# Performance work log

Hardware: AMD Instinct MI355X
Metric: run time of the kernel (lower is better)

The kernel has to match this reference:

```python
import jax, jax.numpy as jnp
import numpy as np

SHIFTS = (1, 2, 4, 8)


def _base_kernels():
    # 8 directional contrast kernels (center minus one neighbor), as in the torch module
    d1 = np.array([[[-1, 0, 0], [0, 1, 0], [0, 0, 0]],
                   [[0, -1, 0], [0, 1, 0], [0, 0, 0]],
                   [[0, 0, -1], [0, 1, 0], [0, 0, 0]],
                   [[0, 0, 0], [0, 1, -1], [0, 0, 0]]], dtype=np.float32)
    d2 = d1[:, ::-1, ::-1].copy()
    delta = np.concatenate([d1, d2], axis=0)            # (8,3,3) kernel*_1
    su0 = np.ones((3, 3), np.float32) / 8.0             # original kernel_su
    ce = np.zeros((3, 3), np.float32); ce[1, 1] = 1.0   # kernel_ce
    k2 = (delta - ce) * (9.0 / 8.0) + su0               # (8,3,3) kernel*_2
    su_f = su0 * (7.0 / 8.0); su_f[1, 1] = 1.0 / 8.0    # mutated kernel_su used for cen_x
    return jnp.asarray(delta), jnp.asarray(k2), jnp.asarray(su_f), jnp.asarray(ce)


def _dwconv(x, w, dil, groups):
    # depthwise 3x3 dilated conv, padding='same' (stride 1)
    return jax.lax.conv_general_dilated(
        x, w, window_strides=(1, 1), padding='SAME',
        rhs_dilation=(dil, dil),
        dimension_numbers=('NCHW', 'OIHW', 'NCHW'),
        feature_group_count=groups)


def setup_inputs() -> dict:
    key = jax.random.key(0)
    ks = jax.random.split(key, 6)
    B, C, Wd, Ht = 8, 16, 192, 192
    H, T, OC = 4, 64, 32
    hid = T // H  # 16
    return {
        'cen': jax.random.normal(ks[0], (B, C, Wd, Ht), jnp.float32),
        'wq': jax.random.normal(ks[1], (H, hid, C), jnp.float32) * 0.1,
        'wk': jax.random.normal(ks[2], (H, 8 * hid, 8 * C), jnp.float32) * 0.05,
        'wv': jax.random.normal(ks[3], (H, 8 * hid, 8 * C), jnp.float32) * 0.05,
        'sum_w': jnp.full((H, C), 0.5, jnp.float32),  # Parameter(ones)*0.5
        'w_out': jax.random.normal(ks[4], (OC, T), jnp.float32) * 0.1,
        'gamma': jnp.ones((OC,), jnp.float32),
        'beta': jnp.zeros((OC,), jnp.float32),
    }


def reference(cen, wq, wk, wv, sum_w, w_out, gamma, beta):
    delta, k2, su_f, ce = _base_kernels()
    B, C, Wd, Ht = cen.shape
    H = len(SHIFTS)
    hid = wq.shape[1]
    N = Wd * Ht  # self.area
    qs, ks_, vs = [], [], []
    for i, s in enumerate(SHIFTS):
        sw = sum_w[i]  # (C,) per-channel blend weight
        # center-smoothing kernel: kernel_su*(1-sw) + sw*kernel_ce
        w_cen = (su_f[None] * (1.0 - sw)[:, None, None]
                 + ce[None] * sw[:, None, None])[:, None]          # (C,1,3,3)
        cen_x = _dwconv(cen, w_cen, s, C)                           # (B,C,Wd,Ht)
        # 8 blended contrast kernels: k1*(1-sw) + k2*sw, per channel
        w_sur = (delta[None] * (1.0 - sw)[:, None, None, None]
                 + k2[None] * sw[:, None, None, None]).reshape(C * 8, 1, 3, 3)
        sur = _dwconv(cen, w_sur, s, C)                             # (B, C*8, Wd, Ht), channel-major
        # reorder to torch cat order: [k0 all C, k1 all C, ...]
        sur = sur.reshape(B, C, 8, Wd, Ht).transpose(0, 2, 1, 3, 4).reshape(B, 8 * C, Wd, Ht)
        qs.append(jnp.einsum('oc,bchw->bohw', wq[i], cen_x).reshape(B, hid, N))
        ks_.append(jnp.einsum('oc,bchw->bohw', wk[i], sur).reshape(B, 8 * hid, N))
        vs.append(jnp.einsum('oc,bchw->bohw', wv[i], sur).reshape(B, 8 * hid, N))
    Q = jnp.stack(qs, 1)   # (B,H,hid,N)
    K = jnp.stack(ks_, 1)  # (B,H,8*hid,N)
    V = jnp.stack(vs, 1)   # (B,H,8*hid,N)
    # F.normalize over spatial dim (channel attention)
    Qn = Q / jnp.maximum(jnp.linalg.norm(Q, axis=-1, keepdims=True), 1e-12)
    Kn = K / jnp.maximum(jnp.linalg.norm(K, axis=-1, keepdims=True), 1e-12)
    score = jnp.einsum('bhqn,bhkn->bhqk', Qn, Kn) / jnp.sqrt(jnp.float32(N))
    # InstanceNorm2d(num_heads), affine=False, biased var
    m = score.mean(axis=(-2, -1), keepdims=True)
    v = score.var(axis=(-2, -1), keepdims=True)
    score = (score - m) / jnp.sqrt(v + 1e-5)
    attn = jax.nn.softmax(score, axis=-1)
    out = jnp.einsum('bhqk,bhkn->bhqn', attn, V).reshape(B, H * hid, Wd, Ht)  # (B,T,Wd,Ht)
    # out_conv: 1x1 conv + BatchNorm2d (train-mode batch stats) + ReLU
    y = jnp.einsum('oc,bchw->bohw', w_out, out)
    mu = y.mean(axis=(0, 2, 3), keepdims=True)
    var = y.var(axis=(0, 2, 3), keepdims=True)
    y = (y - mu) / jnp.sqrt(var + 1e-5) * gamma[None, :, None, None] + beta[None, :, None, None]
    return jax.nn.relu(y)
```

## Files before the change

kernel.cpp:

```cpp
#include <hip/hip_runtime.h>
#include <hip/hip_bf16.h>

typedef __hip_bfloat16 bf16;
typedef unsigned short u16;
typedef u16 u16x8 __attribute__((ext_vector_type(8)));
typedef __bf16 bf16x8 __attribute__((ext_vector_type(8)));
typedef float f32x4 __attribute__((ext_vector_type(4)));

#define NPIX 36864
#define NTOT 9437184
#define BNPIX 294912.0f

__device__ __forceinline__ float cvt(float v){ return v; }
__device__ __forceinline__ float cvt(bf16 v){ return __bfloat162float(v); }
__device__ __forceinline__ void stv(float* p, float v){ *p = v; }
__device__ __forceinline__ void stv(bf16* p, float v){ *p = __float2bfloat16(v); }
__device__ __forceinline__ u16 f2us(float v){ bf16 b = __float2bfloat16(v); u16 u; __builtin_memcpy(&u,&b,2); return u; }
__device__ __forceinline__ float us2f(u16 v){ unsigned u = ((unsigned)v)<<16; float f; __builtin_memcpy(&f,&u,4); return f; }
__device__ __forceinline__ void fence(){ __builtin_amdgcn_sched_barrier(0); }

__global__ void k0_detect(const unsigned* __restrict__ gamma_raw, int* __restrict__ mode)
{
    if (threadIdx.x == 0) mode[0] = (gamma_raw[0] == 0x3F803F80u) ? 1 : 0;
}

struct K1S { u16 F[144*128]; };

__device__ __forceinline__ void flushU(const f32x4& v, int A, int B, float* __restrict__ g, int ln, int lg)
{
    #pragma unroll
    for (int r = 0; r < 4; ++r)
        atomicAdd(&g[(A*16 + lg*4 + r)*144 + B*16 + ln], v[r]);
}

template<typename T>
__device__ __forceinline__ void ldseg(const T* p, bool pred, float* o)
{
    if constexpr (sizeof(T) == 2){
        u16x8 v = {0,0,0,0,0,0,0,0};
        if (pred) v = *(const u16x8*)p;
        #pragma unroll
        for (int i = 0; i < 8; ++i) o[i] = us2f(v[i]);
    } else {
        float4 a = {0,0,0,0}, b = {0,0,0,0};
        if (pred){ a = ((const float4*)p)[0]; b = ((const float4*)p)[1]; }
        o[0]=a.x; o[1]=a.y; o[2]=a.z; o[3]=a.w; o[4]=b.x; o[5]=b.y; o[6]=b.z; o[7]=b.w;
    }
}

template<typename T, int S_, int H>
__device__ __forceinline__ void k1_phase(const T* __restrict__ cen, const T* __restrict__ sumw,
                                         float* __restrict__ gram, K1S& S, int bx, int b)
{
    const int tid = threadIdx.x;
    const int lane = tid & 63;
    const int w = tid >> 6;
    const int ln = lane & 15, lg = lane >> 4;
    const int c = tid & 15, glocal = tid >> 4;

    f32x4 acc[12];
    #pragma unroll
    for (int j = 0; j < 12; ++j) acc[j] = (f32x4){0.f,0.f,0.f,0.f};

    const float swc = cvt(sumw[H*16 + c]);
    const T* cc = cen + ((size_t)(b*16 + c))*NPIX;
    const int gs = glocal ^ c;

    #pragma unroll 1
    for (int ck = 0; ck < 6; ++ck){
        const int gg = (bx*6 + ck)*16 + glocal;
        const int row = gg/24;
        const int colb = (gg - row*24)*8;
        float w3[3][24];
        #pragma unroll
        for (int rr = 0; rr < 3; ++rr){
            int r2 = row + (rr-1)*S_;
            bool rok = (unsigned)r2 < 192u;
            const T* rp = cc + r2*192 + colb;
            ldseg(rp-8, rok && (colb != 0),   &w3[rr][0]);
            ldseg(rp,   rok,                  &w3[rr][8]);
            ldseg(rp+8, rok && (colb != 184), &w3[rr][16]);
        }
        u16x8 o[9];
        #pragma unroll
        for (int j = 0; j < 8; ++j){
            float t00=w3[0][8+j-S_], t01=w3[0][8+j], t02=w3[0][8+j+S_];
            float t10=w3[1][8+j-S_], x0 =w3[1][8+j], t12=w3[1][8+j+S_];
            float t20=w3[2][8+j-S_], t21=w3[2][8+j], t22=w3[2][8+j+S_];
            float S9 = ((t00+t01)+(t02+t10))+((x0+t12)+(t20+t21))+t22;
            float cenx = (1.f-swc)*(S9*(7.f/64.f) + x0*(1.f/64.f)) + swc*x0;
            float cf = 1.f + swc*0.125f;
            float bs = swc*(S9*0.125f - 1.125f*x0);
            o[0][j] = f2us(cenx);
            o[1][j] = f2us(cf*(x0-t00)+bs);
            o[2][j] = f2us(cf*(x0-t01)+bs);
            o[3][j] = f2us(cf*(x0-t02)+bs);
            o[4][j] = f2us(cf*(x0-t12)+bs);
            o[5][j] = f2us(cf*(x0-t22)+bs);
            o[6][j] = f2us(cf*(x0-t21)+bs);
            o[7][j] = f2us(cf*(x0-t20)+bs);
            o[8][j] = f2us(cf*(x0-t10)+bs);
        }
        *(u16x8*)&S.F[c*128 + gs*8] = o[0];
        #pragma unroll
        for (int d = 0; d < 8; ++d)
            *(u16x8*)&S.F[(16 + d*16 + c)*128 + gs*8] = o[d+1];
        fence();
        __syncthreads();
        fence();
        #pragma unroll
        for (int ks = 0; ks < 4; ++ks){
            bf16x8 fg[9];
            #pragma unroll
            for (int blk = 0; blk < 9; ++blk){
                u16x8 raw = *(const u16x8*)&S.F[(blk*16+ln)*128 + ((ks*4+lg) ^ ln)*8];
                fg[blk] = __builtin_bit_cast(bf16x8, raw);
            }
            #define MT(j,A,B) acc[j] = __builtin_amdgcn_mfma_f32_16x16x32_bf16(fg[A], fg[B], acc[j], 0, 0, 0)
            if (w == 0){
                MT(0,0,0); MT(1,0,1); MT(2,0,2); MT(3,0,3); MT(4,0,4); MT(5,0,5);
                MT(6,0,6); MT(7,0,7); MT(8,0,8); MT(9,4,4); MT(10,4,5);
            } else if (w == 1){
                MT(0,1,1); MT(1,1,2); MT(2,1,3); MT(3,1,4); MT(4,1,5); MT(5,1,6);
                MT(6,1,7); MT(7,1,8); MT(8,4,6); MT(9,4,7); MT(10,4,8);
            } else if (w == 2){
                MT(0,2,2); MT(1,2,3); MT(2,2,4); MT(3,2,5); MT(4,2,6); MT(5,2,7);
                MT(6,2,8); MT(7,5,5); MT(8,5,6); MT(9,5,7); MT(10,5,8);
            } else {
                MT(0,3,3); MT(1,3,4); MT(2,3,5); MT(3,3,6); MT(4,3,7); MT(5,3,8);
                MT(6,6,6); MT(7,6,7); MT(8,6,8); MT(9,7,7); MT(10,7,8); MT(11,8,8);
            }
            #undef MT
        }
        fence();
        __syncthreads();
        fence();
    }

    float* g = gram + (size_t)(b*4 + H) * 20736;
    if (w == 0){
        flushU(acc[0],0,0,g,ln,lg); flushU(acc[1],0,1,g,ln,lg); flushU(acc[2],0,2,g,ln,lg);
        flushU(acc[3],0,3,g,ln,lg); flushU(acc[4],0,4,g,ln,lg); flushU(acc[5],0,5,g,ln,lg);
        flushU(acc[6],0,6,g,ln,lg); flushU(acc[7],0,7,g,ln,lg); flushU(acc[8],0,8,g,ln,lg);
        flushU(acc[9],4,4,g,ln,lg); flushU(acc[10],4,5,g,ln,lg);
    } else if (w == 1){
        flushU(acc[0],1,1,g,ln,lg); flushU(acc[1],1,2,g,ln,lg); flushU(acc[2],1,3,g,ln,lg);
        flushU(acc[3],1,4,g,ln,lg); flushU(acc[4],1,5,g,ln,lg); flushU(acc[5],1,6,g,ln,lg);
        flushU(acc[6],1,7,g,ln,lg); flushU(acc[7],1,8,g,ln,lg); flushU(acc[8],4,6,g,ln,lg);
        flushU(acc[9],4,7,g,ln,lg); flushU(acc[10],4,8,g,ln,lg);
    } else if (w == 2){
        flushU(acc[0],2,2,g,ln,lg); flushU(acc[1],2,3,g,ln,lg); flushU(acc[2],2,4,g,ln,lg);
        flushU(acc[3],2,5,g,ln,lg); flushU(acc[4],2,6,g,ln,lg); flushU(acc[5],2,7,g,ln,lg);
        flushU(acc[6],2,8,g,ln,lg); flushU(acc[7],5,5,g,ln,lg); flushU(acc[8],5,6,g,ln,lg);
        flushU(acc[9],5,7,g,ln,lg); flushU(acc[10],5,8,g,ln,lg);
    } else {
        flushU(acc[0],3,3,g,ln,lg); flushU(acc[1],3,4,g,ln,lg); flushU(acc[2],3,5,g,ln,lg);
        flushU(acc[3],3,6,g,ln,lg); flushU(acc[4],3,7,g,ln,lg); flushU(acc[5],3,8,g,ln,lg);
        flushU(acc[6],6,6,g,ln,lg); flushU(acc[7],6,7,g,ln,lg); flushU(acc[8],6,8,g,ln,lg);
        flushU(acc[9],7,7,g,ln,lg); flushU(acc[10],7,8,g,ln,lg); flushU(acc[11],8,8,g,ln,lg);
    }
}

template<typename T>
__device__ __forceinline__ void k1_all(const T* __restrict__ cen, const T* __restrict__ sumw,
                                       float* __restrict__ gram, K1S& S)
{
    const int bid = blockIdx.x;
    const int b = bid & 7;
    const int bx = bid >> 3;
    k1_phase<T,1,0>(cen, sumw, gram, S, bx, b);
    k1_phase<T,2,1>(cen, sumw, gram, S, bx, b);
    k1_phase<T,4,2>(cen, sumw, gram, S, bx, b);
    k1_phase<T,8,3>(cen, sumw, gram, S, bx, b);
}

__global__ __launch_bounds__(256,2)
void k1_gram(const void* cen, const void* sumw, float* gram, const int* mode)
{
    __shared__ K1S S;
    if (mode[0]) k1_all<bf16>((const bf16*)cen, (const bf16*)sumw, gram, S);
    else         k1_all<float>((const float*)cen, (const float*)sumw, gram, S);
}

__global__ __launch_bounds__(256,1)
void k1_sym(float* __restrict__ gram)
{
    float* g = gram + (size_t)blockIdx.x * 20736;
    for (int e = threadIdx.x; e < 20736; e += 256){
        int r = e/144, c = e - r*144;
        if ((r>>4) > (c>>4)) g[e] = g[c*144 + r];
    }
}

struct K2aS { float wkr[16][129]; float part[16][17]; };

template<typename T>
__device__ __forceinline__ void k2a_body(const float* __restrict__ gram, const T* __restrict__ wk,
                                         float* __restrict__ knorm, K2aS& S)
{
    const int bh = blockIdx.y, h = bh & 3;
    const int k0 = blockIdx.x * 16;
    const int tid = threadIdx.x;
    for (int idx = tid; idx < 2048; idx += 256){
        int k = idx >> 7, c = idx & 127;
        S.wkr[k][c] = cvt(wk[h*16384 + (k0+k)*128 + c]);
    }
    __syncthreads();
    const int kl = tid & 15, pp = tid >> 4;
    const float* g = gram + (size_t)bh*20736;
    float acc = 0.f;
    for (int c = pp*8; c < pp*8+8; ++c){
        const float* grow = g + (16+c)*144 + 16;
        float s_ = 0.f;
        for (int c2 = 0; c2 < 128; ++c2) s_ += S.wkr[kl][c2]*grow[c2];
        acc += S.wkr[kl][c]*s_;
    }
    S.part[pp][kl] = acc;
    __syncthreads();
    if (tid < 16){
        float t = 0.f;
        #pragma unroll
        for (int p2 = 0; p2 < 16; ++p2) t += S.part[p2][tid];
        knorm[bh*128 + k0 + tid] = sqrtf(fmaxf(t, 0.f));
    }
}

__global__ __launch_bounds__(256,1)
void k2a_knorm(const float* gram, const void* wk, float* knorm, const int* mode)
{
    __shared__ K2aS S;
    if (mode[0]) k2a_body<bf16>(gram, (const bf16*)wk, knorm, S);
    else         k2a_body<float>(gram, (const float*)wk, knorm, S);
}

struct K2bS {
    float sc[16][128];
    float tmve[16][128];
    float wqf[16][16];
    float qn[16];
    float red1[4], red2[4];
    float m_s, i_s;
};

template<typename T>
__device__ __forceinline__ void k2b_body(const float* __restrict__ gram, const float* __restrict__ knorm,
                                         const T* __restrict__ wq, const T* __restrict__ wk,
                                         const T* __restrict__ wv, const T* __restrict__ wout,
                                         u16* __restrict__ weff2b, K2bS& S)
{
    const int bh = blockIdx.x, h = bh & 3;
    const int tid = threadIdx.x;
    const float* g = gram + (size_t)bh*20736;

    S.wqf[tid>>4][tid&15] = cvt(wq[h*256 + tid]);
    __syncthreads();

    if (tid < 16){
        float acc = 0.f;
        for (int c = 0; c < 16; ++c){
            const float* gr = g + c*144;
            float s_ = 0.f;
            for (int c2 = 0; c2 < 16; ++c2) s_ += S.wqf[tid][c2]*gr[c2];
            acc += S.wqf[tid][c]*s_;
        }
        S.qn[tid] = sqrtf(fmaxf(acc, 0.f));
    }
    for (int e = tid; e < 2048; e += 256){
        int q = e>>7, c2 = e&127;
        float s_ = 0.f;
        #pragma unroll
        for (int c = 0; c < 16; ++c) s_ += S.wqf[q][c]*g[c*144 + 16 + c2];
        S.tmve[q][c2] = s_;
    }
    __syncthreads();
    for (int e = tid; e < 2048; e += 256){
        int q = e>>7, k = e&127;
        const T* wkrow = wk + h*16384 + k*128;
        float s_ = 0.f;
        for (int c2 = 0; c2 < 128; ++c2) s_ += S.tmve[q][c2]*cvt(wkrow[c2]);
        float nq = fmaxf(S.qn[q], 1e-12f);
        float nk = fmaxf(knorm[bh*128+k], 1e-12f);
        S.sc[q][k] = s_/(nq*nk) * (1.f/192.f);
    }
    __syncthreads();
    float s1 = 0.f, s2 = 0.f;
    for (int e = tid; e < 2048; e += 256){ float v = S.sc[e>>7][e&127]; s1 += v; s2 += v*v; }
    #pragma unroll
    for (int o = 1; o < 64; o <<= 1){ s1 += __shfl_xor(s1,o); s2 += __shfl_xor(s2,o); }
    if ((tid&63) == 0){ S.red1[tid>>6] = s1; S.red2[tid>>6] = s2; }
    __syncthreads();
    if (tid == 0){
        float a = S.red1[0]+S.red1[1]+S.red1[2]+S.red1[3];
        float qq = S.red2[0]+S.red2[1]+S.red2[2]+S.red2[3];
        float m = a*(1.f/2048.f);
        float var = qq*(1.f/2048.f) - m*m;
        S.m_s = m; S.i_s = rsqrtf(var + 1e-5f);
    }
    __syncthreads();
    {
        float mm = S.m_s, ii = S.i_s;
        for (int e = tid; e < 2048; e += 256){ int q = e>>7, k = e&127; S.sc[q][k] = (S.sc[q][k]-mm)*ii; }
    }
    __syncthreads();
    if (tid < 16){
        float mx = -1e30f;
        for (int k = 0; k < 128; ++k) mx = fmaxf(mx, S.sc[tid][k]);
        float sm = 0.f;
        for (int k = 0; k < 128; ++k){ float e_ = __expf(S.sc[tid][k]-mx); S.sc[tid][k] = e_; sm += e_; }
        float inv = 1.f/sm;
        for (int k = 0; k < 128; ++k) S.sc[tid][k] *= inv;
    }
    __syncthreads();
    for (int e = tid; e < 2048; e += 256){
        int q = e>>7, c = e&127;
        float s_ = 0.f;
        for (int k = 0; k < 128; ++k) s_ += S.sc[q][k]*cvt(wv[h*16384 + k*128 + c]);
        S.tmve[q][c] = s_;
    }
    __syncthreads();
    for (int e = tid; e < 4096; e += 256){
        int f = e>>5, oc = e&31;
        float s_ = 0.f;
        #pragma unroll
        for (int q = 0; q < 16; ++q) s_ += cvt(wout[oc*64 + h*16 + q])*S.tmve[q][f];
        int d = f >> 4, c = f & 15;
        weff2b[(size_t)bh*4096 + oc*128 + c*8 + d] = f2us(s_);
    }
}

__global__ __launch_bounds__(256,1)
void k2b_attn(const float* gram, const float* knorm, const void* wq, const void* wk,
              const void* wv, const void* wout, u16* weff2b, const int* mode)
{
    __shared__ K2bS S;
    if (mode[0]) k2b_body<bf16>(gram, knorm, (const bf16*)wq, (const bf16*)wk, (const bf16*)wv, (const bf16*)wout, weff2b, S);
    else         k2b_body<float>(gram, knorm, (const float*)wq, (const float*)wk, (const float*)wv, (const float*)wout, weff2b, S);
}

struct K3S { u16 feat[128*128]; u16 wlds[32*128]; };

__device__ __forceinline__ int kkey(int x){ return ((x>>3) ^ x) & 15; }

template<typename T, int S_, int H>
__device__ __forceinline__ void k3_step(const T* __restrict__ cc, float swc,
                                        const u16* __restrict__ wsrc,
                                        int row, int colb, int p0, int c,
                                        int tid, int ln, int lg, int wm, int wn,
                                        f32x4* acc, K3S& S)
{
    #pragma unroll
    for (int i = 0; i < 2; ++i){
        int e = tid + 256*i;
        int oc = e >> 4, slot = e & 15;
        u16x8 v = *(const u16x8*)&wsrc[oc*128 + slot*8];
        *(u16x8*)&S.wlds[oc*128 + ((slot ^ kkey(oc)) & 15)*8] = v;
    }
    float w3[3][24];
    #pragma unroll
    for (int rr = 0; rr < 3; ++rr){
        int r2 = row + (rr-1)*S_;
        bool rok = (unsigned)r2 < 192u;
        const T* rp = cc + r2*192 + colb;
        ldseg(rp-8, rok && (colb != 0),   &w3[rr][0]);
        ldseg(rp,   rok,                  &w3[rr][8]);
        ldseg(rp+8, rok && (colb != 184), &w3[rr][16]);
    }
    #pragma unroll
    for (int j = 0; j < 8; ++j){
        float t00=w3[0][8+j-S_], t01=w3[0][8+j], t02=w3[0][8+j+S_];
        float t10=w3[1][8+j-S_], x0 =w3[1][8+j], t12=w3[1][8+j+S_];
        float t20=w3[2][8+j-S_], t21=w3[2][8+j], t22=w3[2][8+j+S_];
        float S9 = ((t00+t01)+(t02+t10))+((x0+t12)+(t20+t21))+t22;
        float cf = 1.f + swc*0.125f;
        float bs = swc*(S9*0.125f - 1.125f*x0);
        u16x8 pk;
        pk[0] = f2us(cf*(x0-t00)+bs);
        pk[1] = f2us(cf*(x0-t01)+bs);
        pk[2] = f2us(cf*(x0-t02)+bs);
        pk[3] = f2us(cf*(x0-t12)+bs);
        pk[4] = f2us(cf*(x0-t22)+bs);
        pk[5] = f2us(cf*(x0-t21)+bs);
        pk[6] = f2us(cf*(x0-t20)+bs);
        pk[7] = f2us(cf*(x0-t10)+bs);
        int p = p0 + j;
        *(u16x8*)&S.feat[p*128 + ((c ^ kkey(p)) & 15)*8] = pk;
    }
    fence();
    __syncthreads();
    fence();
    const int ocl = wm*16 + ln;
    #pragma unroll
    for (int kt = 0; kt < 4; ++kt){
        const int slot = kt*4 + lg;
        u16x8 araw = *(const u16x8*)&S.wlds[ocl*128 + ((slot ^ kkey(ocl)) & 15)*8];
        bf16x8 a = __builtin_bit_cast(bf16x8, araw);
        #pragma unroll
        for (int nt = 0; nt < 4; ++nt){
            const int pixl = wn*64 + nt*16 + ln;
            u16x8 braw = *(const u16x8*)&S.feat[pixl*128 + ((slot ^ kkey(pixl)) & 15)*8];
            bf16x8 bb = __builtin_bit_cast(bf16x8, braw);
            acc[nt] = __builtin_amdgcn_mfma_f32_16x16x32_bf16(a, bb, acc[nt], 0, 0, 0);
        }
    }
    fence();
    __syncthreads();
    fence();
}

template<typename T, bool YF32>
__device__ __forceinline__ void k3_body(const T* __restrict__ cen, const T* __restrict__ sumw,
                                        const u16* __restrict__ weff2b, float* __restrict__ ysum,
                                        T* __restrict__ outp, float* __restrict__ yf, K3S& S)
{
    const int bid = blockIdx.x;
    const int b = bid & 7;
    const int k = bid >> 3;
    const int cs = k % 3;
    const int rp = k / 3;
    const int tid = threadIdx.x;
    const int lane = tid & 63;
    const int w = tid >> 6;
    const int wm = w >> 1, wn = w & 1;
    const int ln = lane & 15, lg = lane >> 4;
    const int c = tid >> 4, g = tid & 15;
    const int grow = g >> 3, gcol = g & 7;

    const int row = rp*2 + grow;
    const int colb = cs*64 + gcol*8;
    const int p0 = grow*64 + gcol*8;
    const T* cc = cen + ((size_t)(b*16 + c))*NPIX;

    f32x4 acc[4];
    #pragma unroll
    for (int nt = 0; nt < 4; ++nt) acc[nt] = (f32x4){0.f,0.f,0.f,0.f};

    const u16* wb = weff2b + (size_t)(b*4)*4096;
    k3_step<T,1,0>(cc, cvt(sumw[ 0 + c]), wb,          row, colb, p0, c, tid, ln, lg, wm, wn, acc, S);
    k3_step<T,2,1>(cc, cvt(sumw[16 + c]), wb + 4096,   row, colb, p0, c, tid, ln, lg, wm, wn, acc, S);
    k3_step<T,4,2>(cc, cvt(sumw[32 + c]), wb + 8192,   row, colb, p0, c, tid, ln, lg, wm, wn, acc, S);
    k3_step<T,8,3>(cc, cvt(sumw[48 + c]), wb + 12288,  row, colb, p0, c, tid, ln, lg, wm, wn, acc, S);

    const int oc0 = wm*16 + lg*4;
    #pragma unroll
    for (int nt = 0; nt < 4; ++nt){
        const int pixl = wn*64 + nt*16 + ln;
        const int gr = rp*2 + (pixl>>6);
        const int gc = cs*64 + (pixl & 63);
        #pragma unroll
        for (int r = 0; r < 4; ++r){
            const size_t a = (size_t)b*32*NPIX + (size_t)(oc0+r)*NPIX + (size_t)gr*192 + gc;
            if (YF32) yf[a] = acc[nt][r];
            else      stv(&outp[a], acc[nt][r]);
        }
    }
    float* ys = ysum + (rp & 7)*64;
    #pragma unroll
    for (int r = 0; r < 4; ++r){
        float s1 = 0.f, s2 = 0.f;
        #pragma unroll
        for (int nt = 0; nt < 4; ++nt){ s1 += acc[nt][r]; s2 += acc[nt][r]*acc[nt][r]; }
        #pragma unroll
        for (int o = 1; o < 16; o <<= 1){ s1 += __shfl_xor(s1,o); s2 += __shfl_xor(s2,o); }
        if (ln == 0){ atomicAdd(&ys[oc0+r], s1); atomicAdd(&ys[32+oc0+r], s2); }
    }
}

template<bool YF32>
__global__ __launch_bounds__(256,4)
void k3_out(const void* cen, const void* sumw, const u16* weff2b, float* ysum,
            void* outp, float* yf, const int* mode)
{
    __shared__ K3S S;
    if (mode[0]) k3_body<bf16,YF32>((const bf16*)cen, (const bf16*)sumw, weff2b, ysum, (bf16*)outp, yf, S);
    else         k3_body<float,YF32>((const float*)cen, (const float*)sumw, weff2b, ysum, (float*)outp, yf, S);
}

__global__ void k4_stats(const float* __restrict__ ysum, const void* gamma_,
                         const void* beta_, float* __restrict__ ss, const int* mode)
{
    int oc = threadIdx.x;
    if (oc < 32){
        float gv, bv;
        if (mode[0]){ gv = cvt(((const bf16*)gamma_)[oc]); bv = cvt(((const bf16*)beta_)[oc]); }
        else        { gv = ((const float*)gamma_)[oc];     bv = ((const float*)beta_)[oc]; }
        float s1 = 0.f, s2 = 0.f;
        #pragma unroll
        for (int sl = 0; sl < 8; ++sl){ s1 += ysum[sl*64 + oc]; s2 += ysum[sl*64 + 32 + oc]; }
        float m = s1 / BNPIX;
        float var = s2 / BNPIX - m*m;
        float istd = rsqrtf(var + 1e-5f);
        float scl = istd * gv;
        ss[oc] = scl;
        ss[32+oc] = bv - m*scl;
    }
}

template<typename T, bool YF32>
__device__ __forceinline__ void k5_body(const float* __restrict__ ss, const float* __restrict__ yf, T* __restrict__ out)
{
    size_t i0 = ((size_t)blockIdx.x*256 + threadIdx.x)*8;
    if (i0 >= (size_t)NTOT) return;
    int oc = (int)((i0/NPIX) & 31);
    float scl = ss[oc], shf = ss[32+oc];
    float v[8];
    if (YF32){
        const float4* p = (const float4*)(yf + i0);
        float4 a = p[0], b = p[1];
        v[0]=a.x; v[1]=a.y; v[2]=a.z; v[3]=a.w; v[4]=b.x; v[5]=b.y; v[6]=b.z; v[7]=b.w;
    } else {
        if constexpr (sizeof(T) == 2){
            u16x8 a = *(const u16x8*)(out + i0);
            #pragma unroll
            for (int j = 0; j < 8; ++j) v[j] = us2f(a[j]);
        } else {
            const float4* p = (const float4*)((const float*)out + i0);
            float4 a = p[0], b = p[1];
            v[0]=a.x; v[1]=a.y; v[2]=a.z; v[3]=a.w; v[4]=b.x; v[5]=b.y; v[6]=b.z; v[7]=b.w;
        }
    }
    if constexpr (sizeof(T) == 2){
        u16x8 r;
        #pragma unroll
        for (int j = 0; j < 8; ++j){ float y = fmaxf(v[j]*scl + shf, 0.f); r[j] = f2us(y); }
        *(u16x8*)(out + i0) = r;
    } else {
        float4 r0, r1;
        r0.x = fmaxf(v[0]*scl+shf,0.f); r0.y = fmaxf(v[1]*scl+shf,0.f);
        r0.z = fmaxf(v[2]*scl+shf,0.f); r0.w = fmaxf(v[3]*scl+shf,0.f);
        r1.x = fmaxf(v[4]*scl+shf,0.f); r1.y = fmaxf(v[5]*scl+shf,0.f);
        r1.z = fmaxf(v[6]*scl+shf,0.f); r1.w = fmaxf(v[7]*scl+shf,0.f);
        ((float4*)((float*)out + i0))[0] = r0;
        ((float4*)((float*)out + i0))[1] = r1;
    }
}

template<bool YF32>
__global__ __launch_bounds__(256,2)
void k5_norm(const float* ss, const float* yf, void* out, const int* mode)
{
    if (mode[0]) k5_body<bf16,YF32>(ss, yf, (bf16*)out);
    else         k5_body<float,YF32>(ss, yf, (float*)out);
}

extern "C" void kernel_launch(void* const* d_in, const int* in_sizes, int n_in,
                              void* d_out, int out_size, void* d_ws, size_t ws_size,
                              hipStream_t stream)
{
    (void)in_sizes; (void)n_in; (void)out_size;
    const void* cen   = d_in[0];
    const void* wq    = d_in[1];
    const void* wk    = d_in[2];
    const void* wv    = d_in[3];
    const void* sumw  = d_in[4];
    const void* wout  = d_in[5];
    const void* gamma = d_in[6];
    const void* beta  = d_in[7];
    float* ws = (float*)d_ws;

    float* gram   = ws;
    u16*   weff2b = (u16*)(ws + 663552);
    float* knorm  = ws + 794624;
    float* ysum   = ws + 798720;
    float* sshift = ws + 799232;
    int*   modep  = (int*)(ws + 799296);
    float* yf     = ws + 799360;
    const bool yf32 = (ws_size >= (size_t)(799360 + NTOT) * 4);

    k0_detect<<<1, 64, 0, stream>>>((const unsigned*)gamma, modep);
    hipMemsetAsync(gram, 0, 663552*sizeof(float), stream);
    hipMemsetAsync(ysum, 0, 512*sizeof(float), stream);

    k1_gram<<<dim3(384), 256, 0, stream>>>(cen, sumw, gram, modep);
    k1_sym<<<32, 256, 0, stream>>>(gram);

    k2a_knorm<<<dim3(8,32), 256, 0, stream>>>(gram, wk, knorm, modep);
    k2b_attn<<<dim3(32), 256, 0, stream>>>(gram, knorm, wq, wk, wv, wout, weff2b, modep);
    if (yf32){
        k3_out<true><<<dim3(2304), 256, 0, stream>>>(cen, sumw, weff2b, ysum, d_out, yf, modep);
        k4_stats<<<1, 64, 0, stream>>>(ysum, gamma, beta, sshift, modep);
        k5_norm<true><<<4608, 256, 0, stream>>>(sshift, yf, d_out, modep);
    } else {
        k3_out<false><<<dim3(2304), 256, 0, stream>>>(cen, sumw, weff2b, ysum, d_out, yf, modep);
        k4_stats<<<1, 64, 0, stream>>>(ysum, gamma, beta, sshift, modep);
        k5_norm<false><<<4608, 256, 0, stream>>>(sshift, yf, d_out, modep);
    }
}
```

Measured before the change: 301.8 us.

## Replace gram atomic flush with per-block partial stores and a reduce kernel

Each k1_gram block now writes its upper-triangle gram tiles to a private partial buffer instead of atomically adding into the shared gram. A new k1_red kernel sums the 48 spatial-chunk partials per tile and writes both the tile and its symmetric mirror. This removes the gram memset and the k1_sym pass. The cost is a large extra workspace buffer that is written once and read once. The old atomic path stays as a fallback when the workspace is too small, and the workspace offsets are repacked to make room.

```diff
diff --git a/kernel.cpp b/kernel.cpp
--- a/kernel.cpp
+++ b/kernel.cpp
@@ -19,6 +19,9 @@
 __device__ __forceinline__ float us2f(u16 v){ unsigned u = ((unsigned)v)<<16; float f; __builtin_memcpy(&f,&u,4); return f; }
 __device__ __forceinline__ void fence(){ __builtin_amdgcn_sched_barrier(0); }
 
+__constant__ int tA[45] = {0,0,0,0,0,0,0,0,0,4,4, 1,1,1,1,1,1,1,1,4,4,4, 2,2,2,2,2,2,2,5,5,5,5, 3,3,3,3,3,3,6,6,6,7,7,8};
+__constant__ int tB[45] = {0,1,2,3,4,5,6,7,8,4,5, 1,2,3,4,5,6,7,8,6,7,8, 2,3,4,5,6,7,8,5,6,7,8, 3,4,5,6,7,8,6,7,8,7,8,8};
+
 __global__ void k0_detect(const unsigned* __restrict__ gamma_raw, int* __restrict__ mode)
 {
     if (threadIdx.x == 0) mode[0] = (gamma_raw[0] == 0x3F803F80u) ? 1 : 0;
@@ -48,9 +51,10 @@
     }
 }
 
-template<typename T, int S_, int H>
+template<typename T, int S_, int H, bool STORE>
 __device__ __forceinline__ void k1_phase(const T* __restrict__ cen, const T* __restrict__ sumw,
-                                         float* __restrict__ gram, K1S& S, int bx, int b)
+                                         float* __restrict__ gram, float* __restrict__ gpart,
+                                         K1S& S, int bx, int b)
 {
     const int tid = threadIdx.x;
     const int lane = tid & 63;
@@ -137,49 +141,81 @@
         fence();
     }
 
-    float* g = gram + (size_t)(b*4 + H) * 20736;
-    if (w == 0){
-        flushU(acc[0],0,0,g,ln,lg); flushU(acc[1],0,1,g,ln,lg); flushU(acc[2],0,2,g,ln,lg);
-        flushU(acc[3],0,3,g,ln,lg); flushU(acc[4],0,4,g,ln,lg); flushU(acc[5],0,5,g,ln,lg);
-        flushU(acc[6],0,6,g,ln,lg); flushU(acc[7],0,7,g,ln,lg); flushU(acc[8],0,8,g,ln,lg);
-        flushU(acc[9],4,4,g,ln,lg); flushU(acc[10],4,5,g,ln,lg);
-    } else if (w == 1){
-        flushU(acc[0],1,1,g,ln,lg); flushU(acc[1],1,2,g,ln,lg); flushU(acc[2],1,3,g,ln,lg);
-        flushU(acc[3],1,4,g,ln,lg); flushU(acc[4],1,5,g,ln,lg); flushU(acc[5],1,6,g,ln,lg);
-        flushU(acc[6],1,7,g,ln,lg); flushU(acc[7],1,8,g,ln,lg); flushU(acc[8],4,6,g,ln,lg);
-        flushU(acc[9],4,7,g,ln,lg); flushU(acc[10],4,8,g,ln,lg);
-    } else if (w == 2){
-        flushU(acc[0],2,2,g,ln,lg); flushU(acc[1],2,3,g,ln,lg); flushU(acc[2],2,4,g,ln,lg);
-        flushU(acc[3],2,5,g,ln,lg); flushU(acc[4],2,6,g,ln,lg); flushU(acc[5],2,7,g,ln,lg);
-        flushU(acc[6],2,8,g,ln,lg); flushU(acc[7],5,5,g,ln,lg); flushU(acc[8],5,6,g,ln,lg);
-        flushU(acc[9],5,7,g,ln,lg); flushU(acc[10],5,8,g,ln,lg);
+    if (STORE){
+        float* gp = gpart + (((size_t)(bx*8 + b)*4 + H)*45)*256;
+        const int base = w*11;
+        const int nt = (w == 3) ? 12 : 11;
+        #pragma unroll
+        for (int j = 0; j < 12; ++j){
+            if (j < nt){
+                float* tp = gp + (base + j)*256 + lg*64 + ln;
+                #pragma unroll
+                for (int r = 0; r < 4; ++r) tp[r*16] = acc[j][r];
+            }
+        }
     } else {
-        flushU(acc[0],3,3,g,ln,lg); flushU(acc[1],3,4,g,ln,lg); flushU(acc[2],3,5,g,ln,lg);
-        flushU(acc[3],3,6,g,ln,lg); flushU(acc[4],3,7,g,ln,lg); flushU(acc[5],3,8,g,ln,lg);
-        flushU(acc[6],6,6,g,ln,lg); flushU(acc[7],6,7,g,ln,lg); flushU(acc[8],6,8,g,ln,lg);
-        flushU(acc[9],7,7,g,ln,lg); flushU(acc[10],7,8,g,ln,lg); flushU(acc[11],8,8,g,ln,lg);
-    }
-}
-
-template<typename T>
+        float* g = gram + (size_t)(b*4 + H) * 20736;
+        if (w == 0){
+            flushU(acc[0],0,0,g,ln,lg); flushU(acc[1],0,1,g,ln,lg); flushU(acc[2],0,2,g,ln,lg);
+            flushU(acc[3],0,3,g,ln,lg); flushU(acc[4],0,4,g,ln,lg); flushU(acc[5],0,5,g,ln,lg);
+            flushU(acc[6],0,6,g,ln,lg); flushU(acc[7],0,7,g,ln,lg); flushU(acc[8],0,8,g,ln,lg);
+            flushU(acc[9],4,4,g,ln,lg); flushU(acc[10],4,5,g,ln,lg);
+        } else if (w == 1){
+            flushU(acc[0],1,1,g,ln,lg); flushU(acc[1],1,2,g,ln,lg); flushU(acc[2],1,3,g,ln,lg);
+            flushU(acc[3],1,4,g,ln,lg); flushU(acc[4],1,5,g,ln,lg); flushU(acc[5],1,6,g,ln,lg);
+            flushU(acc[6],1,7,g,ln,lg); flushU(acc[7],1,8,g,ln,lg); flushU(acc[8],4,6,g,ln,lg);
+            flushU(acc[9],4,7,g,ln,lg); flushU(acc[10],4,8,g,ln,lg);
+        } else if (w == 2){
+            flushU(acc[0],2,2,g,ln,lg); flushU(acc[1],2,3,g,ln,lg); flushU(acc[2],2,4,g,ln,lg);
+            flushU(acc[3],2,5,g,ln,lg); flushU(acc[4],2,6,g,ln,lg); flushU(acc[5],2,7,g,ln,lg);
+            flushU(acc[6],2,8,g,ln,lg); flushU(acc[7],5,5,g,ln,lg); flushU(acc[8],5,6,g,ln,lg);
+            flushU(acc[9],5,7,g,ln,lg); flushU(acc[10],5,8,g,ln,lg);
+        } else {
+            flushU(acc[0],3,3,g,ln,lg); flushU(acc[1],3,4,g,ln,lg); flushU(acc[2],3,5,g,ln,lg);
+            flushU(acc[3],3,6,g,ln,lg); flushU(acc[4],3,7,g,ln,lg); flushU(acc[5],3,8,g,ln,lg);
+            flushU(acc[6],6,6,g,ln,lg); flushU(acc[7],6,7,g,ln,lg); flushU(acc[8],6,8,g,ln,lg);
+            flushU(acc[9],7,7,g,ln,lg); flushU(acc[10],7,8,g,ln,lg); flushU(acc[11],8,8,g,ln,lg);
+        }
+    }
+}
+
+template<typename T, bool STORE>
 __device__ __forceinline__ void k1_all(const T* __restrict__ cen, const T* __restrict__ sumw,
-                                       float* __restrict__ gram, K1S& S)
+                                       float* __restrict__ gram, float* __restrict__ gpart, K1S& S)
 {
     const int bid = blockIdx.x;
     const int b = bid & 7;
     const int bx = bid >> 3;
-    k1_phase<T,1,0>(cen, sumw, gram, S, bx, b);
-    k1_phase<T,2,1>(cen, sumw, gram, S, bx, b);
-    k1_phase<T,4,2>(cen, sumw, gram, S, bx, b);
-    k1_phase<T,8,3>(cen, sumw, gram, S, bx, b);
-}
-
+    k1_phase<T,1,0,STORE>(cen, sumw, gram, gpart, S, bx, b);
+    k1_phase<T,2,1,STORE>(cen, sumw, gram, gpart, S, bx, b);
+    k1_phase<T,4,2,STORE>(cen, sumw, gram, gpart, S, bx, b);
+    k1_phase<T,8,3,STORE>(cen, sumw, gram, gpart, S, bx, b);
+}
+
+template<bool STORE>
 __global__ __launch_bounds__(256,2)
-void k1_gram(const void* cen, const void* sumw, float* gram, const int* mode)
+void k1_gram(const void* cen, const void* sumw, float* gram, float* gpart, const int* mode)
 {
     __shared__ K1S S;
-    if (mode[0]) k1_all<bf16>((const bf16*)cen, (const bf16*)sumw, gram, S);
-    else         k1_all<float>((const float*)cen, (const float*)sumw, gram, S);
+    if (mode[0]) k1_all<bf16,STORE>((const bf16*)cen, (const bf16*)sumw, gram, gpart, S);
+    else         k1_all<float,STORE>((const float*)cen, (const float*)sumw, gram, gpart, S);
+}
+
+__global__ __launch_bounds__(256,4)
+void k1_red(const float* __restrict__ gpart, float* __restrict__ gram)
+{
+    const int t = blockIdx.x;
+    const int bh = blockIdx.y;
+    const int e = threadIdx.x;
+    const float* p = gpart + (size_t)bh*45*256 + (size_t)t*256 + e;
+    float s = 0.f;
+    #pragma unroll 4
+    for (int sx = 0; sx < 48; ++sx) s += p[(size_t)sx*32*45*256];
+    const int A = tA[t], B = tB[t];
+    const int rr = e >> 4, cc2 = e & 15;
+    float* g = gram + (size_t)bh*20736;
+    g[(A*16+rr)*144 + B*16 + cc2] = s;
+    if (A != B) g[(B*16+cc2)*144 + A*16 + rr] = s;
 }
 
 __global__ __launch_bounds__(256,1)
@@ -559,19 +595,28 @@
 
     float* gram   = ws;
     u16*   weff2b = (u16*)(ws + 663552);
-    float* knorm  = ws + 794624;
-    float* ysum   = ws + 798720;
-    float* sshift = ws + 799232;
-    int*   modep  = (int*)(ws + 799296);
-    float* yf     = ws + 799360;
-    const bool yf32 = (ws_size >= (size_t)(799360 + NTOT) * 4);
+    float* knorm  = ws + 729088;
+    float* ysum   = ws + 733184;
+    float* sshift = ws + 733696;
+    int*   modep  = (int*)(ws + 733760);
+    float* gpart  = ws + 733776;
+    const size_t GPART_F = (size_t)1536*45*256;
+    const bool store = (ws_size >= (733776 + GPART_F) * 4);
+    float* yf = store ? (gpart + GPART_F) : gpart;
+    const size_t yf_end = ((size_t)(yf - ws) + NTOT) * 4;
+    const bool yf32 = (ws_size >= yf_end);
 
     k0_detect<<<1, 64, 0, stream>>>((const unsigned*)gamma, modep);
-    hipMemsetAsync(gram, 0, 663552*sizeof(float), stream);
     hipMemsetAsync(ysum, 0, 512*sizeof(float), stream);
 
-    k1_gram<<<dim3(384), 256, 0, stream>>>(cen, sumw, gram, modep);
-    k1_sym<<<32, 256, 0, stream>>>(gram);
+    if (store){
+        k1_gram<true><<<dim3(384), 256, 0, stream>>>(cen, sumw, gram, gpart, modep);
+        k1_red<<<dim3(45,32), 256, 0, stream>>>(gpart, gram);
+    } else {
+        hipMemsetAsync(gram, 0, 663552*sizeof(float), stream);
+        k1_gram<false><<<dim3(384), 256, 0, stream>>>(cen, sumw, gram, gpart, modep);
+        k1_sym<<<32, 256, 0, stream>>>(gram);
+    }
 
     k2a_knorm<<<dim3(8,32), 256, 0, stream>>>(gram, wk, knorm, modep);
     k2b_attn<<<dim3(32), 256, 0, stream>>>(gram, knorm, wq, wk, wv, wout, weff2b, modep);
```

After: 277.4 us. -8.1%, faster.
